# Performance work log

Measured on AMD Instinct MI355X. Metric: run time of the kernel, lower is better.

The kernel has to match this reference:

```python
import jax, jax.numpy as jnp
import numpy as np

B, D, U = 4096, 1024, 1024

def cumax(a):
    # Faithful to source: softmax over last axis, cumsum over axis 0 (TF defaults).
    return jnp.cumsum(jax.nn.softmax(a, axis=-1), axis=0)

def setup_inputs() -> dict:
    key = jax.random.key(0)
    ks = jax.random.split(key, 21)
    names = ['inputs', 'hidden_prev', 'cell_prev',
             'Wf', 'Uf', 'bf', 'Wi', 'Ui', 'bi', 'Wo', 'Uo', 'bo',
             'Wc', 'Uc', 'bc', 'Wft', 'Uft', 'bft', 'Wit', 'Uit', 'bit']
    shapes = [(B, D), (B, U), (B, U)] + [(D, U), (U, U), (U,)] * 6
    scales = [1.0, 1.0, 1.0] + [0.05, 0.05, 0.05] * 6  # random_normal init ~ small stddev
    return {n: jax.random.normal(k, s, dtype=jnp.float32) * sc
            for n, k, s, sc in zip(names, ks, shapes, scales)}

def reference(inputs, hidden_prev, cell_prev,
              Wf, Uf, bf, Wi, Ui, bi, Wo, Uo, bo,
              Wc, Uc, bc, Wft, Uft, bft, Wit, Uit, bit):
    # Fuse the 12 small GEMMs into 2 big ones: [B,D]@[D,6U] and [B,U]@[U,6U]
    W_all = jnp.concatenate([Wf, Wi, Wo, Wc, Wft, Wit], axis=1)   # [D, 6U]
    U_all = jnp.concatenate([Uf, Ui, Uo, Uc, Uft, Uit], axis=1)   # [U, 6U]
    b_all = jnp.concatenate([bf, bi, bo, bc, bft, bit], axis=0)   # [6U]
    pre = inputs @ W_all + hidden_prev @ U_all + b_all            # [B, 6U]
    zf, zi, zo, zc, zft, zit = [pre[:, j*U:(j+1)*U] for j in range(6)]

    f = jax.nn.sigmoid(zf)
    i = jax.nn.sigmoid(zi)
    o = jax.nn.sigmoid(zo)
    c_hat = jnp.tanh(zc)
    f_tilde = cumax(zft)
    i_tilde = 1.0 - cumax(zit)

    omega = f_tilde * i_tilde
    f_hat = f * omega + (f_tilde - omega)
    i_hat = i * omega + (i_tilde - omega)
    cell = f_hat * cell_prev + i_hat * c_hat
    hidden = o * jnp.tanh(cell)
    return hidden, cell
```

## Files before the change

### kernel.cpp

```cpp
#include <hip/hip_runtime.h>
#include <cstdint>
#include <cstddef>


typedef _Float16 half8  __attribute__((ext_vector_type(8)));
typedef _Float16 half4v __attribute__((ext_vector_type(4)));
typedef float f32x4 __attribute__((ext_vector_type(4)));

__device__ __forceinline__ void async16(const _Float16* g, _Float16* l) {
  __builtin_amdgcn_global_load_lds(
      (const __attribute__((address_space(1))) void*)g,
      (__attribute__((address_space(3))) void*)l, 16, 0, 0);
}

struct Ptrs12 { const float* p[12]; };
struct Ptrs6  { const float* p[6];  };

__global__ void prep(const float* __restrict__ X, const float* __restrict__ H,
                     Ptrs12 w, Ptrs6 bs,
                     _Float16* __restrict__ Ahi, _Float16* __restrict__ Bhi,
                     float* __restrict__ b_all) {
  __shared__ float tile[64][65];
  const int blk = blockIdx.x;
  const int t = threadIdx.x;
  if (blk < 8192) {
    size_t base = ((size_t)blk * 256 + t) * 4;
    int k = (int)(base & 2047);
    size_t b = base >> 11;
    const float* src = (k < 1024) ? (X + b * 1024 + k) : (H + b * 1024 + (k - 1024));
    float4 v = *(const float4*)src;
    half4v hi = { (_Float16)v.x, (_Float16)v.y, (_Float16)v.z, (_Float16)v.w };
    *(half4v*)(Ahi + base) = hi;
  } else if (blk < 11264) {
    int bb = blk - 8192;
    int mat = bb >> 8;
    int tl = bb & 255;
    int tr = tl >> 4, tc = tl & 15;
    int g = mat >> 1, s = mat & 1;
    const float* src = w.p[mat];
    int col = t & 63, r0 = t >> 6;
#pragma unroll
    for (int i = 0; i < 16; i++) {
      int row = i * 4 + r0;
      tile[row][col] = src[(size_t)(tr * 64 + row) * 1024 + tc * 64 + col];
    }
    __syncthreads();
    int c2 = t >> 2, kseg = t & 3;
    half8 v0, v1;
#pragma unroll
    for (int j = 0; j < 8; j++) {
      v0[j] = (_Float16)(tile[kseg * 16 + j][c2] * 64.0f);
      v1[j] = (_Float16)(tile[kseg * 16 + 8 + j][c2] * 64.0f);
    }
    size_t n  = (size_t)g * 1024 + tc * 64 + c2;
    size_t kk = (size_t)s * 1024 + tr * 64 + kseg * 16;
    *(half8*)(Bhi + n * 2048 + kk) = v0;
    *(half8*)(Bhi + n * 2048 + kk + 8) = v1;
  } else {
    int n = (blk - 11264) * 256 + t;
    b_all[n] = bs.p[n >> 10][n & 1023];
  }
}


#define LGKM0 asm volatile("s_waitcnt lgkmcnt(0)" ::: "memory")

__device__ __forceinline__ void wg_barrier() {
  __builtin_amdgcn_s_barrier();
  asm volatile("" ::: "memory");
}

#define PHASE(TT, MH, NH, STAGE_STMT, WAIT_STMT)                               \
  {                                                                            \
    const _Float16* bufA_ = lds + ((TT) & 1) * 24576 + (MH) * 4096;            \
    const _Float16* bufB_ = lds + ((TT) & 1) * 24576 + 8192 + (NH) * 8192;     \
    half8 af[2][2], bf[2][2];                                                  \
    _Pragma("unroll")                                                          \
    for (int f = 0; f < 2; f++) {                                              \
      int r = wm * 32 + f * 16 + frow;                                         \
      _Pragma("unroll")                                                        \
      for (int ks = 0; ks < 2; ks++)                                           \
        af[f][ks] = *(const half8*)(bufA_ + r * 64 +                           \
                                    (((ks * 4 + kgrp) ^ (r & 7)) * 8));        \
    }                                                                          \
    _Pragma("unroll")                                                          \
    for (int g = 0; g < 2; g++) {                                              \
      int r = wn * 32 + g * 16 + frow;                                         \
      _Pragma("unroll")                                                        \
      for (int ks = 0; ks < 2; ks++)                                           \
        bf[g][ks] = *(const half8*)(bufB_ + r * 64 +                           \
                                    (((ks * 4 + kgrp) ^ (r & 7)) * 8));        \
    }                                                                          \
    STAGE_STMT;                                                                \
    LGKM0;                                                                     \
    WAIT_STMT;                                                                 \
    wg_barrier();                                                              \
    __builtin_amdgcn_s_setprio(1);                                             \
    _Pragma("unroll")                                                          \
    for (int f = 0; f < 2; f++)                                                \
      _Pragma("unroll")                                                        \
      for (int g = 0; g < 2; g++)                                              \
        _Pragma("unroll")                                                      \
        for (int ks = 0; ks < 2; ks++)                                         \
          acc[(MH) * 2 + f][(NH) * 2 + g] =                                    \
              __builtin_amdgcn_mfma_f32_16x16x32_f16(                          \
                  af[f][ks], bf[g][ks], acc[(MH) * 2 + f][(NH) * 2 + g],       \
                  0, 0, 0);                                                    \
    __builtin_amdgcn_s_setprio(0);                                             \
  }

__global__ __launch_bounds__(512, 2) void gemm_8ph(
    const _Float16* __restrict__ Ah, const _Float16* __restrict__ Bh,
    const float* __restrict__ b_all, _Float16* __restrict__ pre16) {
  __shared__ __attribute__((aligned(16))) _Float16 lds[49152];

  const int bid = blockIdx.x;
  const int swz = (bid & 7) * 96 + (bid >> 3);
  const int nTile = swz / 32;
  const int mTile = swz % 32;

  const int t = threadIdx.x;
  const int lane = t & 63;
  const int wave = t >> 6;
  const int wm = wave >> 2, wn = wave & 3;
  const int kgrp = lane >> 4, frow = lane & 15;

  const _Float16* Abase = Ah + (size_t)mTile * 128 * 2048;
  const _Float16* Bbase = Bh + (size_t)nTile * 256 * 2048;

  f32x4 acc[4][4] = {};

  auto stageA = [&](int kt, int mh) {
    int r = t >> 3, k8 = t & 7;
    int xs = k8 ^ (r & 7);
    const _Float16* g = Abase + (size_t)(mh * 64 + r) * 2048 + kt * 64 + xs * 8;
    _Float16* l = lds + (kt & 1) * 24576 + mh * 4096 + t * 8;
    async16(g, l);
  };
  auto stageB = [&](int kt, int nh) {
#pragma unroll
    for (int q = 0; q < 2; q++) {
      int s = q * 512 + t;
      int r = s >> 3, k8 = s & 7;
      int xs = k8 ^ (r & 7);
      const _Float16* g = Bbase + (size_t)(nh * 128 + r) * 2048 + kt * 64 + xs * 8;
      _Float16* l = lds + (kt & 1) * 24576 + 8192 + nh * 8192 + s * 8;
      async16(g, l);
    }
  };

  stageA(0, 0); stageB(0, 0); stageA(0, 1); stageB(0, 1);
  stageA(1, 0); stageB(1, 0);
  asm volatile("s_waitcnt vmcnt(3)" ::: "memory");
  wg_barrier();

#pragma unroll 2
  for (int T = 0; T < 32; T++) {
    PHASE(T, 0, 0, { if (T + 1 < 32) stageA(T + 1, 1); }, {});
    PHASE(T, 0, 1, { if (T + 1 < 32) stageB(T + 1, 1); }, {});
    PHASE(T, 1, 0, { if (T + 2 < 32) stageA(T + 2, 0); }, {});
    PHASE(T, 1, 1, { if (T + 2 < 32) stageB(T + 2, 0); },
          { if (T < 30) { asm volatile("s_waitcnt vmcnt(3)" ::: "memory"); }
            else        { asm volatile("s_waitcnt vmcnt(0)" ::: "memory"); } });
  }

  const float inv64 = 1.0f / 64.0f;
  const int cb = nTile * 256;
  float bias[4];
#pragma unroll
  for (int nj = 0; nj < 4; nj++) {
    int col = (nj >> 1) * 128 + wn * 32 + (nj & 1) * 16 + frow;
    bias[nj] = b_all[cb + col];
  }
#pragma unroll
  for (int mi = 0; mi < 4; mi++) {
#pragma unroll
    for (int nj = 0; nj < 4; nj++) {
      int row = (mi >> 1) * 64 + wm * 32 + (mi & 1) * 16 + kgrp * 4;
      int col = (nj >> 1) * 128 + wn * 32 + (nj & 1) * 16 + frow;
#pragma unroll
      for (int j = 0; j < 4; j++)
        lds[(row + j) * 264 + col] =
            (_Float16)(acc[mi][nj][j] * inv64 + bias[nj]);
    }
  }
  __syncthreads();
#pragma unroll
  for (int rr = 0; rr < 8; rr++) {
    int L = rr * 4096 + t * 8;
    int row = L >> 8, col = L & 255;
    half8 v = *(const half8*)(lds + row * 264 + col);
    *(half8*)(pre16 + (size_t)(mTile * 128 + row) * 6144 + cb + col) = v;
  }
}

__global__ void softmax_partials(_Float16* __restrict__ pre16, f32x4* __restrict__ part4) {
  __shared__ float wsum[4][1024];
  int m = blockIdx.x >> 9;
  int ch = blockIdx.x & 511;
  int t = threadIdx.x;
  int wave = t >> 6, lane = t & 63;
  f32x4 colacc[4] = {};
  for (int rr = 0; rr < 2; rr++) {
    int b = ch * 8 + wave * 2 + rr;
    _Float16* row = pre16 + (size_t)b * 6144 + (4 + m) * 1024;
    f32x4 v[4];
    float mx = -3.4e38f;
#pragma unroll
    for (int j = 0; j < 4; j++) {
      half4v h = *(const half4v*)(row + lane * 4 + 256 * j);
      v[j] = f32x4{ (float)h[0], (float)h[1], (float)h[2], (float)h[3] };
      mx = fmaxf(mx, fmaxf(fmaxf(v[j][0], v[j][1]), fmaxf(v[j][2], v[j][3])));
    }
#pragma unroll
    for (int off = 32; off > 0; off >>= 1) mx = fmaxf(mx, __shfl_xor(mx, off, 64));
    float sum = 0.f;
#pragma unroll
    for (int j = 0; j < 4; j++)
#pragma unroll
      for (int q = 0; q < 4; q++) { v[j][q] = __expf(v[j][q] - mx); sum += v[j][q]; }
#pragma unroll
    for (int off = 32; off > 0; off >>= 1) sum += __shfl_xor(sum, off, 64);
    float inv = 1.f / sum;
#pragma unroll
    for (int j = 0; j < 4; j++) {
      v[j] *= inv;
      half4v h = { (_Float16)v[j][0], (_Float16)v[j][1], (_Float16)v[j][2], (_Float16)v[j][3] };
      *(half4v*)(row + lane * 4 + 256 * j) = h;
      colacc[j] += v[j];
    }
  }
#pragma unroll
  for (int j = 0; j < 4; j++)
    *(f32x4*)(&wsum[wave][lane * 4 + 256 * j]) = colacc[j];
  __syncthreads();
  f32x4 s = *(const f32x4*)(&wsum[0][t * 4]);
  s += *(const f32x4*)(&wsum[1][t * 4]);
  s += *(const f32x4*)(&wsum[2][t * 4]);
  s += *(const f32x4*)(&wsum[3][t * 4]);
  part4[((size_t)m * 256 + t) * 512 + ch] = s;
}

__global__ void scan_partials(const f32x4* __restrict__ part4, f32x4* __restrict__ off4) {
  int gidx = blockIdx.x * 4 + (threadIdx.x >> 6);
  int lane = threadIdx.x & 63;
  size_t base = (size_t)gidx * 512;
  f32x4 v[8];
  f32x4 s = {};
#pragma unroll
  for (int j = 0; j < 8; j++) {
    v[j] = part4[base + lane * 8 + j];
    s += v[j];
  }
  f32x4 incl = s;
#pragma unroll
  for (int off = 1; off < 64; off <<= 1) {
    f32x4 o;
#pragma unroll
    for (int q = 0; q < 4; q++) o[q] = __shfl_up(incl[q], off, 64);
    if (lane >= off) incl += o;
  }
  f32x4 run = incl - s;
#pragma unroll
  for (int j = 0; j < 8; j++) {
    off4[base + lane * 8 + j] = run;
    run += v[j];
  }
}

__global__ void onlstm_final(const _Float16* __restrict__ pre16,
                             const float* __restrict__ cprev, const f32x4* __restrict__ off4,
                             float* __restrict__ out) {
  int ch = blockIdx.x;
  int c4 = threadIdx.x;
  int c = c4 * 4;
  f32x4 runf = off4[(size_t)c4 * 512 + ch];
  f32x4 runi = off4[(size_t)(256 + c4) * 512 + ch];
  for (int r = 0; r < 8; r++) {
    int b = ch * 8 + r;
    const _Float16* row = pre16 + (size_t)b * 6144;
    half4v zf = *(const half4v*)(row + c);
    half4v zi = *(const half4v*)(row + 1024 + c);
    half4v zo = *(const half4v*)(row + 2048 + c);
    half4v zc = *(const half4v*)(row + 3072 + c);
    half4v pf = *(const half4v*)(row + 4096 + c);
    half4v pi = *(const half4v*)(row + 5120 + c);
    f32x4 cp = *(const f32x4*)(cprev + (size_t)b * 1024 + c);
    f32x4 hid, cel;
#pragma unroll
    for (int q = 0; q < 4; q++) {
      runf[q] += (float)pf[q];
      runi[q] += (float)pi[q];
      float ft = runf[q], it = 1.f - runi[q];
      float f  = 1.f / (1.f + __expf(-(float)zf[q]));
      float ii = 1.f / (1.f + __expf(-(float)zi[q]));
      float o  = 1.f / (1.f + __expf(-(float)zo[q]));
      float chat = tanhf((float)zc[q]);
      float omega = ft * it;
      float fhat = f * omega + (ft - omega);
      float ihat = ii * omega + (it - omega);
      float cell = fhat * cp[q] + ihat * chat;
      hid[q] = o * tanhf(cell);
      cel[q] = cell;
    }
    *(f32x4*)(out + (size_t)b * 1024 + c) = hid;
    *(f32x4*)(out + (size_t)4194304 + (size_t)b * 1024 + c) = cel;
  }
}

extern "C" void kernel_launch(void* const* d_in, const int* in_sizes, int n_in,
                              void* d_out, int out_size, void* d_ws, size_t ws_size,
                              hipStream_t stream) {
  const float* X = (const float*)d_in[0];
  const float* H = (const float*)d_in[1];
  const float* C = (const float*)d_in[2];

  char* ws = (char*)d_ws;
  _Float16* pre16 = (_Float16*)(ws);
  _Float16* Ahi   = (_Float16*)(ws + 50331648);
  _Float16* Bhi   = (_Float16*)(ws + 67108864);
  float*    b_all = (float*)(ws + 92274688);
  f32x4*    part4 = (f32x4*)(ws + 92299264);
  f32x4*    off4  = (f32x4*)(ws + 96493568);

  Ptrs12 w;
  for (int g = 0; g < 6; g++) {
    w.p[2 * g]     = (const float*)d_in[3 + 3 * g];
    w.p[2 * g + 1] = (const float*)d_in[4 + 3 * g];
  }
  Ptrs6 bs;
  for (int g = 0; g < 6; g++) bs.p[g] = (const float*)d_in[5 + 3 * g];

  prep<<<11288, 256, 0, stream>>>(X, H, w, bs, Ahi, Bhi, b_all);
  gemm_8ph<<<768, 512, 0, stream>>>(Ahi, Bhi, b_all, pre16);
  softmax_partials<<<1024, 256, 0, stream>>>(pre16, part4);
  scan_partials<<<128, 256, 0, stream>>>(part4, off4);
  onlstm_final<<<512, 256, 0, stream>>>(pre16, C, off4, (float*)d_out);
}
```

Before: 329.8 us.

## Replace four-phase double-buffered GEMM with triple-buffered ring and single barrier per tile

Restructures the fp16 MFMA GEMM main loop from four sub-phases per k-tile, each with its own barrier and partial A/B staging, to a three-slot LDS ring. Each iteration stages the whole tile two steps ahead and synchronises once per k-tile, between the two k-halves of the MFMA work. Each wave now owns a contiguous 64x64 output block. The aim is to cut barrier and wait overhead and give loads more time in flight. The cost is LDS per block growing from 96KB to 144KB and more fragment registers held live.

```diff
diff --git a/kernel.cpp b/kernel.cpp
--- a/kernel.cpp
+++ b/kernel.cpp
@@ -70,49 +70,10 @@
   asm volatile("" ::: "memory");
 }
 
-#define PHASE(TT, MH, NH, STAGE_STMT, WAIT_STMT)                               \
-  {                                                                            \
-    const _Float16* bufA_ = lds + ((TT) & 1) * 24576 + (MH) * 4096;            \
-    const _Float16* bufB_ = lds + ((TT) & 1) * 24576 + 8192 + (NH) * 8192;     \
-    half8 af[2][2], bf[2][2];                                                  \
-    _Pragma("unroll")                                                          \
-    for (int f = 0; f < 2; f++) {                                              \
-      int r = wm * 32 + f * 16 + frow;                                         \
-      _Pragma("unroll")                                                        \
-      for (int ks = 0; ks < 2; ks++)                                           \
-        af[f][ks] = *(const half8*)(bufA_ + r * 64 +                           \
-                                    (((ks * 4 + kgrp) ^ (r & 7)) * 8));        \
-    }                                                                          \
-    _Pragma("unroll")                                                          \
-    for (int g = 0; g < 2; g++) {                                              \
-      int r = wn * 32 + g * 16 + frow;                                         \
-      _Pragma("unroll")                                                        \
-      for (int ks = 0; ks < 2; ks++)                                           \
-        bf[g][ks] = *(const half8*)(bufB_ + r * 64 +                           \
-                                    (((ks * 4 + kgrp) ^ (r & 7)) * 8));        \
-    }                                                                          \
-    STAGE_STMT;                                                                \
-    LGKM0;                                                                     \
-    WAIT_STMT;                                                                 \
-    wg_barrier();                                                              \
-    __builtin_amdgcn_s_setprio(1);                                             \
-    _Pragma("unroll")                                                          \
-    for (int f = 0; f < 2; f++)                                                \
-      _Pragma("unroll")                                                        \
-      for (int g = 0; g < 2; g++)                                              \
-        _Pragma("unroll")                                                      \
-        for (int ks = 0; ks < 2; ks++)                                         \
-          acc[(MH) * 2 + f][(NH) * 2 + g] =                                    \
-              __builtin_amdgcn_mfma_f32_16x16x32_f16(                          \
-                  af[f][ks], bf[g][ks], acc[(MH) * 2 + f][(NH) * 2 + g],       \
-                  0, 0, 0);                                                    \
-    __builtin_amdgcn_s_setprio(0);                                             \
-  }
-
-__global__ __launch_bounds__(512, 2) void gemm_8ph(
+__global__ __launch_bounds__(512, 2) void gemm_ring(
     const _Float16* __restrict__ Ah, const _Float16* __restrict__ Bh,
     const float* __restrict__ b_all, _Float16* __restrict__ pre16) {
-  __shared__ __attribute__((aligned(16))) _Float16 lds[49152];
+  __shared__ __attribute__((aligned(16))) _Float16 lds[73728];
 
   const int bid = blockIdx.x;
   const int swz = (bid & 7) * 96 + (bid >> 3);
@@ -130,54 +91,96 @@
 
   f32x4 acc[4][4] = {};
 
-  auto stageA = [&](int kt, int mh) {
-    int r = t >> 3, k8 = t & 7;
-    int xs = k8 ^ (r & 7);
-    const _Float16* g = Abase + (size_t)(mh * 64 + r) * 2048 + kt * 64 + xs * 8;
-    _Float16* l = lds + (kt & 1) * 24576 + mh * 4096 + t * 8;
-    async16(g, l);
-  };
-  auto stageB = [&](int kt, int nh) {
+  auto stage_tile = [&](int kt, int base) {
 #pragma unroll
     for (int q = 0; q < 2; q++) {
       int s = q * 512 + t;
       int r = s >> 3, k8 = s & 7;
       int xs = k8 ^ (r & 7);
-      const _Float16* g = Bbase + (size_t)(nh * 128 + r) * 2048 + kt * 64 + xs * 8;
-      _Float16* l = lds + (kt & 1) * 24576 + 8192 + nh * 8192 + s * 8;
-      async16(g, l);
+      async16(Abase + (size_t)r * 2048 + kt * 64 + xs * 8, lds + base + s * 8);
+    }
+#pragma unroll
+    for (int q = 0; q < 4; q++) {
+      int s = q * 512 + t;
+      int r = s >> 3, k8 = s & 7;
+      int xs = k8 ^ (r & 7);
+      async16(Bbase + (size_t)r * 2048 + kt * 64 + xs * 8,
+              lds + base + 8192 + s * 8);
     }
   };
 
-  stageA(0, 0); stageB(0, 0); stageA(0, 1); stageB(0, 1);
-  stageA(1, 0); stageB(1, 0);
-  asm volatile("s_waitcnt vmcnt(3)" ::: "memory");
+  int cur = 0, nxt = 24576, nn = 49152;
+
+  stage_tile(0, cur);
+  stage_tile(1, nxt);
+  asm volatile("s_waitcnt vmcnt(6)" ::: "memory");
   wg_barrier();
 
-#pragma unroll 2
   for (int T = 0; T < 32; T++) {
-    PHASE(T, 0, 0, { if (T + 1 < 32) stageA(T + 1, 1); }, {});
-    PHASE(T, 0, 1, { if (T + 1 < 32) stageB(T + 1, 1); }, {});
-    PHASE(T, 1, 0, { if (T + 2 < 32) stageA(T + 2, 0); }, {});
-    PHASE(T, 1, 1, { if (T + 2 < 32) stageB(T + 2, 0); },
-          { if (T < 30) { asm volatile("s_waitcnt vmcnt(3)" ::: "memory"); }
-            else        { asm volatile("s_waitcnt vmcnt(0)" ::: "memory"); } });
-  }
-
+    const _Float16* A_ = lds + cur;
+    const _Float16* B_ = lds + cur + 8192;
+    half8 af[4][2], bf[4][2];
+#pragma unroll
+    for (int mi = 0; mi < 4; mi++) {
+      int r = wm * 64 + mi * 16 + frow;
+#pragma unroll
+      for (int ks = 0; ks < 2; ks++)
+        af[mi][ks] = *(const half8*)(A_ + r * 64 +
+                                     (((ks * 4 + kgrp) ^ (r & 7)) * 8));
+    }
+#pragma unroll
+    for (int nj = 0; nj < 4; nj++) {
+      int r = wn * 64 + nj * 16 + frow;
+#pragma unroll
+      for (int ks = 0; ks < 2; ks++)
+        bf[nj][ks] = *(const half8*)(B_ + r * 64 +
+                                     (((ks * 4 + kgrp) ^ (r & 7)) * 8));
+    }
+    if (T + 2 < 32) stage_tile(T + 2, nn);
+
+    __builtin_amdgcn_s_setprio(1);
+#pragma unroll
+    for (int mi = 0; mi < 4; mi++)
+#pragma unroll
+      for (int nj = 0; nj < 4; nj++)
+        acc[mi][nj] = __builtin_amdgcn_mfma_f32_16x16x32_f16(
+            af[mi][0], bf[nj][0], acc[mi][nj], 0, 0, 0);
+    __builtin_amdgcn_s_setprio(0);
+
+    LGKM0;
+    if (T < 30) {
+      asm volatile("s_waitcnt vmcnt(6)" ::: "memory");
+      wg_barrier();
+    } else if (T == 30) {
+      asm volatile("s_waitcnt vmcnt(0)" ::: "memory");
+      wg_barrier();
+    }
+
+    __builtin_amdgcn_s_setprio(1);
+#pragma unroll
+    for (int mi = 0; mi < 4; mi++)
+#pragma unroll
+      for (int nj = 0; nj < 4; nj++)
+        acc[mi][nj] = __builtin_amdgcn_mfma_f32_16x16x32_f16(
+            af[mi][1], bf[nj][1], acc[mi][nj], 0, 0, 0);
+    __builtin_amdgcn_s_setprio(0);
+
+    int tmp = cur; cur = nxt; nxt = nn; nn = tmp;
+  }
+
+  __syncthreads();
   const float inv64 = 1.0f / 64.0f;
   const int cb = nTile * 256;
   float bias[4];
 #pragma unroll
-  for (int nj = 0; nj < 4; nj++) {
-    int col = (nj >> 1) * 128 + wn * 32 + (nj & 1) * 16 + frow;
-    bias[nj] = b_all[cb + col];
-  }
+  for (int nj = 0; nj < 4; nj++)
+    bias[nj] = b_all[cb + wn * 64 + nj * 16 + frow];
 #pragma unroll
   for (int mi = 0; mi < 4; mi++) {
 #pragma unroll
     for (int nj = 0; nj < 4; nj++) {
-      int row = (mi >> 1) * 64 + wm * 32 + (mi & 1) * 16 + kgrp * 4;
-      int col = (nj >> 1) * 128 + wn * 32 + (nj & 1) * 16 + frow;
+      int row = wm * 64 + mi * 16 + kgrp * 4;
+      int col = wn * 64 + nj * 16 + frow;
 #pragma unroll
       for (int j = 0; j < 4; j++)
         lds[(row + j) * 264 + col] =
@@ -332,7 +335,7 @@
   for (int g = 0; g < 6; g++) bs.p[g] = (const float*)d_in[5 + 3 * g];
 
   prep<<<11288, 256, 0, stream>>>(X, H, w, bs, Ahi, Bhi, b_all);
-  gemm_8ph<<<768, 512, 0, stream>>>(Ahi, Bhi, b_all, pre16);
+  gemm_ring<<<768, 512, 0, stream>>>(Ahi, Bhi, b_all, pre16);
   softmax_partials<<<1024, 256, 0, stream>>>(pre16, part4);
   scan_partials<<<128, 256, 0, stream>>>(part4, off4);
   onlstm_final<<<512, 256, 0, stream>>>(pre16, C, off4, (float*)d_out);
```

Result: faster. 314.4 us (-4.6%).
